# Kernel optimization log

Hardware: AMD Instinct MI355X
Metric: run time of the kernel (lower is better)

Reference implementation:

```python
import jax, jax.numpy as jnp
import numpy as np

D_MODEL = 1024
NUM_HEADS = 16
DEPTH = D_MODEL // NUM_HEADS
B, S = 4, 2048


def setup_inputs() -> dict:
    key = jax.random.key(0)
    ks = jax.random.split(key, 13)
    sd = 1.0 / np.sqrt(D_MODEL)
    inp = {
        "q_in": jax.random.normal(ks[0], (B, S, D_MODEL), jnp.float32),
        "k_in": jax.random.normal(ks[1], (B, S, D_MODEL), jnp.float32),
        "v_in": jax.random.normal(ks[2], (B, S, D_MODEL), jnp.float32),
        # binary padding/causal-style mask: 1 = masked position
        "m_in": (jax.random.uniform(ks[3], (B, 1, S, S)) < 0.1).astype(jnp.float32),
        "Wq": jax.random.normal(ks[4], (D_MODEL, D_MODEL), jnp.float32) * sd,
        "bq": jax.random.normal(ks[5], (D_MODEL,), jnp.float32) * 0.01,
        "Wk": jax.random.normal(ks[6], (D_MODEL, D_MODEL), jnp.float32) * sd,
        "bk": jax.random.normal(ks[7], (D_MODEL,), jnp.float32) * 0.01,
        "Wv": jax.random.normal(ks[8], (D_MODEL, D_MODEL), jnp.float32) * sd,
        "bv": jax.random.normal(ks[9], (D_MODEL,), jnp.float32) * 0.01,
        "Wo": jax.random.normal(ks[10], (D_MODEL, D_MODEL), jnp.float32) * sd,
        "bo": jax.random.normal(ks[11], (D_MODEL,), jnp.float32) * 0.01,
    }
    return inp


def _split(t):
    # [B,S,D] -> [B,H,S,depth]
    b, s, _ = t.shape
    return t.reshape(b, s, NUM_HEADS, DEPTH).transpose(0, 2, 1, 3)


def reference(q_in, k_in, v_in, m_in, Wq, bq, Wk, bk, Wv, bv, Wo, bo):
    # torch Linear: x @ W^T + b
    q = _split(q_in @ Wq.T + bq)
    k = _split(k_in @ Wk.T + bk)
    v = _split(v_in @ Wv.T + bv)
    scale = jnp.sqrt(jnp.asarray(DEPTH, jnp.float32))
    scores = jnp.einsum("bhqd,bhkd->bhqk", q, k) / scale
    scores = scores - m_in * 1e6
    attn = jax.nn.softmax(scores, axis=-1)
    out = jnp.einsum("bhqk,bhkd->bhqd", attn, v)  # [B,H,S,depth]
    out = out.transpose(0, 2, 1, 3).reshape(q_in.shape[0], -1, D_MODEL)
    return out @ Wo.T + bo
```

## Files before the change

kernel.cpp:

```cpp
#include <hip/hip_runtime.h>


typedef __bf16 bf16_t;
typedef __bf16 bf16x4 __attribute__((ext_vector_type(4)));
typedef __bf16 bf16x8 __attribute__((ext_vector_type(8)));
typedef float floatx2 __attribute__((ext_vector_type(2)));
typedef float floatx4 __attribute__((ext_vector_type(4)));
typedef float floatx16 __attribute__((ext_vector_type(16)));

#define DMODEL 1024
#define NHEAD  16
#define DEPTH  64
#define BATCH  4
#define SEQ    2048
#define MROWS  (BATCH * SEQ)

#define QSCALE 0.18033688011112042f

#define GLDS16(gaddr, laddr)                                                   \
  __builtin_amdgcn_global_load_lds(                                            \
      (__attribute__((address_space(1))) void*)(gaddr),                        \
      (__attribute__((address_space(3))) void*)(laddr), 16, 0, 0)

__global__ __launch_bounds__(256) void cvt_weights(
    const float* __restrict__ w0, const float* __restrict__ w1,
    const float* __restrict__ w2, const float* __restrict__ w3,
    bf16_t* __restrict__ out) {
  const int n_per4 = (DMODEL * DMODEL) / 4;
  int idx = blockIdx.x * blockDim.x + threadIdx.x;
  int t = idx / n_per4;
  int e4 = idx - t * n_per4;
  const float* src = (t == 0) ? w0 : (t == 1) ? w1 : (t == 2) ? w2 : w3;
  const float sc = (t == 0) ? QSCALE : 1.0f;
  float4 v = ((const float4*)src)[e4];
  bf16_t* dst = out + (size_t)t * (DMODEL * DMODEL) + (size_t)e4 * 4;
  dst[0] = (bf16_t)(v.x * sc); dst[1] = (bf16_t)(v.y * sc);
  dst[2] = (bf16_t)(v.z * sc); dst[3] = (bf16_t)(v.w * sc);
}

__global__ __launch_bounds__(256) void cvt3(
    const float* __restrict__ q, const float* __restrict__ k,
    const float* __restrict__ v, bf16_t* __restrict__ dst) {
  const size_t n8 = (size_t)MROWS * DMODEL / 8;
  size_t i = (size_t)blockIdx.x * blockDim.x + threadIdx.x;
  int t = (int)(i / n8);
  size_t e = i - (size_t)t * n8;
  const float* src = (t == 0) ? q : (t == 1) ? k : v;
  const float4* s = (const float4*)(src + e * 8);
  float4 f0 = s[0], f1 = s[1];
  bf16x8 o;
  o[0] = (bf16_t)f0.x; o[1] = (bf16_t)f0.y; o[2] = (bf16_t)f0.z; o[3] = (bf16_t)f0.w;
  o[4] = (bf16_t)f1.x; o[5] = (bf16_t)f1.y; o[6] = (bf16_t)f1.z; o[7] = (bf16_t)f1.w;
  *(bf16x8*)(dst + i * 8) = o;
}

__global__ __launch_bounds__(256) void mask_prepack(
    const float* __restrict__ m, unsigned int* __restrict__ M32) {
  size_t t = (size_t)blockIdx.x * blockDim.x + threadIdx.x;
  int lane = (int)(t & 63);
  int it = (int)((t >> 6) & 31);
  int g  = (int)((t >> 11) & 63);
  int b  = (int)(t >> 17);
  int q  = g * 32 + (lane & 31);
  int hi = lane >> 5;
  const float* row = m + ((size_t)b * SEQ + q) * SEQ + it * 64;
  unsigned int bits = 0;
#pragma unroll
  for (int kb = 0; kb < 2; kb++) {
#pragma unroll
    for (int rc = 0; rc < 4; rc++) {
      const int base = kb * 32 + 16 * (rc >> 1) + 8 * hi + 4 * (rc & 1);
      const float4 mv = *(const float4*)(row + base);
      const int bit0 = kb * 16 + rc * 4;
      if (mv.x == 0.f) bits |= 1u << (bit0 + 0);
      if (mv.y == 0.f) bits |= 1u << (bit0 + 1);
      if (mv.z == 0.f) bits |= 1u << (bit0 + 2);
      if (mv.w == 0.f) bits |= 1u << (bit0 + 3);
    }
  }
  M32[t] = bits;
}

__global__ __launch_bounds__(256) void gemm_qkv(
    const bf16_t* __restrict__ Abf3, const bf16_t* __restrict__ Wbf,
    const float* __restrict__ bq, const float* __restrict__ bk,
    const float* __restrict__ bv, bf16_t* __restrict__ Qh,
    bf16_t* __restrict__ Kh, bf16_t* __restrict__ Vth) {
  __shared__ __align__(16) bf16_t As[128 * 64];
  __shared__ __align__(16) bf16_t Bs[128 * 64];
  const int K = DMODEL;
  const int tid = threadIdx.x;
  const int lane = tid & 63;
  const int w = tid >> 6;
  const int quad = lane >> 4;
  const int l16 = lane & 15;
  const int wm = w & 1, wn = w >> 1;
  const int z = blockIdx.z;

  const bf16_t* A = Abf3 + (size_t)z * MROWS * DMODEL;
  const bf16_t* Bt = Wbf + (size_t)z * DMODEL * DMODEL;
  const float* bias = (z == 0) ? bq : (z == 1) ? bk : bv;
  const float bias_scale = (z == 0) ? QSCALE : 1.0f;
  bf16_t* Ov = (z == 0) ? Qh : (z == 1) ? Kh : Vth;

  const int lin = blockIdx.x + 8 * blockIdx.y;
  const int c = lin & 7;
  const int j = lin >> 3;
  const int n0 = (j & 7) * 128;
  const int m0 = ((j >> 3) * 8 + c) * 128;

  const int r8l = lane >> 3;
  const int c8l = (lane & 7) ^ r8l;
  const bf16_t* Ag = A + (size_t)(m0 + w * 32 + r8l) * K + c8l * 8;
  const bf16_t* Bg = Bt + (size_t)(n0 + w * 32 + r8l) * K + c8l * 8;
  char* AsB = (char*)As + (w * 32) * 128;
  char* BsB = (char*)Bs + (w * 32) * 128;

  floatx4 acc[4][4] = {};

  for (int kk = 0; kk < K; kk += 64) {
    __syncthreads();
#pragma unroll
    for (int cl = 0; cl < 4; cl++) {
      GLDS16(Ag + kk + (size_t)(cl * 8) * K, AsB + cl * 8 * 128);
      GLDS16(Bg + kk + (size_t)(cl * 8) * K, BsB + cl * 8 * 128);
    }
    __syncthreads();

#pragma unroll
    for (int kk2 = 0; kk2 < 2; kk2++) {
      bf16x8 af[4], bfr[4];
#pragma unroll
      for (int mi = 0; mi < 4; mi++) {
        const char* Arow = (const char*)As + (wm * 64 + mi * 16 + l16) * 128;
        af[mi] = *(const bf16x8*)(Arow + (((kk2 * 4 + quad) ^ (l16 & 7)) * 16));
      }
#pragma unroll
      for (int ni = 0; ni < 4; ni++) {
        const char* Brow = (const char*)Bs + (wn * 64 + ni * 16 + l16) * 128;
        bfr[ni] = *(const bf16x8*)(Brow + (((kk2 * 4 + quad) ^ (l16 & 7)) * 16));
      }
#pragma unroll
      for (int mi = 0; mi < 4; mi++)
#pragma unroll
        for (int ni = 0; ni < 4; ni++)
          acc[mi][ni] = __builtin_amdgcn_mfma_f32_16x16x32_bf16(af[mi], bfr[ni], acc[mi][ni], 0, 0, 0);
    }
  }

#pragma unroll
  for (int ni = 0; ni < 4; ni++) {
    const int col = n0 + wn * 64 + ni * 16 + l16;
    const float bvl = bias_scale * bias[col];
    const int hh = col >> 6, d = col & (DEPTH - 1);
#pragma unroll
    for (int mi = 0; mi < 4; mi++) {
#pragma unroll
      for (int r = 0; r < 4; r++) {
        const int row = m0 + wm * 64 + mi * 16 + quad * 4 + r;
        const float val = acc[mi][ni][r] + bvl;
        const int bb = row >> 11, s = row & (SEQ - 1);
        if (z != 2) {
          Ov[((((size_t)bb * NHEAD + hh) * SEQ + s) << 6) + d] = (bf16_t)val;
        } else {
          Ov[(((size_t)bb * NHEAD + hh) * DEPTH + d) * SEQ + s] = (bf16_t)val;
        }
      }
    }
  }
}

__global__ __launch_bounds__(256) void gemm_wo(
    const bf16_t* __restrict__ A, const bf16_t* __restrict__ Bt,
    const float* __restrict__ bias, float* __restrict__ Ov,
    int M, int N, int K) {
  __shared__ __align__(16) bf16_t As[128 * 64];
  __shared__ __align__(16) bf16_t Bs[128 * 64];
  const int tid = threadIdx.x;
  const int lane = tid & 63;
  const int w = tid >> 6;
  const int quad = lane >> 4;
  const int l16 = lane & 15;
  const int wm = w & 1, wn = w >> 1;

  const int lin = blockIdx.x + 8 * blockIdx.y;
  const int c = lin & 7;
  const int j = lin >> 3;
  const int n0 = (j & 7) * 128;
  const int m0 = ((j >> 3) * 8 + c) * 128;

  const int r8l = lane >> 3;
  const int c8l = (lane & 7) ^ r8l;
  const bf16_t* Ag = A + (size_t)(m0 + w * 32 + r8l) * K + c8l * 8;
  const bf16_t* Bg = Bt + (size_t)(n0 + w * 32 + r8l) * K + c8l * 8;
  char* AsB = (char*)As + (w * 32) * 128;
  char* BsB = (char*)Bs + (w * 32) * 128;

  floatx4 acc[4][4] = {};

  for (int kk = 0; kk < K; kk += 64) {
    __syncthreads();
#pragma unroll
    for (int cl = 0; cl < 4; cl++) {
      GLDS16(Ag + kk + (size_t)(cl * 8) * K, AsB + cl * 8 * 128);
      GLDS16(Bg + kk + (size_t)(cl * 8) * K, BsB + cl * 8 * 128);
    }
    __syncthreads();

#pragma unroll
    for (int kk2 = 0; kk2 < 2; kk2++) {
      bf16x8 af[4], bfr[4];
#pragma unroll
      for (int mi = 0; mi < 4; mi++) {
        const char* Arow = (const char*)As + (wm * 64 + mi * 16 + l16) * 128;
        af[mi] = *(const bf16x8*)(Arow + (((kk2 * 4 + quad) ^ (l16 & 7)) * 16));
      }
#pragma unroll
      for (int ni = 0; ni < 4; ni++) {
        const char* Brow = (const char*)Bs + (wn * 64 + ni * 16 + l16) * 128;
        bfr[ni] = *(const bf16x8*)(Brow + (((kk2 * 4 + quad) ^ (l16 & 7)) * 16));
      }
#pragma unroll
      for (int mi = 0; mi < 4; mi++)
#pragma unroll
        for (int ni = 0; ni < 4; ni++)
          acc[mi][ni] = __builtin_amdgcn_mfma_f32_16x16x32_bf16(af[mi], bfr[ni], acc[mi][ni], 0, 0, 0);
    }
  }

#pragma unroll
  for (int ni = 0; ni < 4; ni++) {
    const int col = n0 + wn * 64 + ni * 16 + l16;
    const float bv = bias[col];
#pragma unroll
    for (int mi = 0; mi < 4; mi++)
#pragma unroll
      for (int r = 0; r < 4; r++) {
        const int row = m0 + wm * 64 + mi * 16 + quad * 4 + r;
        Ov[(size_t)row * N + col] = acc[mi][ni][r] + bv;
      }
  }
}

__global__ __launch_bounds__(256, 4) void attn_kernel(
    const bf16_t* __restrict__ Qh, const bf16_t* __restrict__ Kh,
    const bf16_t* __restrict__ Vt, const unsigned int* __restrict__ M32,
    bf16_t* __restrict__ O) {
  const int lane = threadIdx.x & 63;
  const int w = __builtin_amdgcn_readfirstlane(threadIdx.x >> 6);
  const int l31 = lane & 31;
  const int hi = lane >> 5;

  const int lin = blockIdx.x + 16 * blockIdx.y + 256 * blockIdx.z;
  const int x8 = lin & 7;
  const int kk = lin >> 3;
  const int qt = kk & 15;
  const int bh = ((kk >> 4) << 3) | x8;
  const int h = bh & 15;
  const int b = bh >> 4;
  const int q0 = qt * 128;

  const bf16_t* Qb = Qh + ((size_t)b * NHEAD + h) * SEQ * DEPTH;
  const bf16_t* Kb = Kh + ((size_t)b * NHEAD + h) * SEQ * DEPTH;
  const bf16_t* Vb = Vt + ((size_t)b * NHEAD + h) * DEPTH * SEQ;
  const unsigned int* Mw =
      M32 + ((size_t)b * 64 + (qt * 4 + w)) * 32 * 64 + lane;

  __shared__ __align__(16) bf16_t Ksm[64 * 64];
  __shared__ __align__(16) bf16_t Vsm[64 * 64];
  __shared__ float Lsm[4][32];

  const int r8 = lane >> 3;
  const int c8 = (lane & 7) ^ r8;
  const int i1 = w * 16 + r8;
  const int i2 = i1 + 8;
  const int lo1 = i1 & 31, lo2 = i2 & 31;
  const int s1 = (i1 & 32) | ((lo1 & ~12) | ((lo1 & 4) << 1) | ((lo1 & 8) >> 1));
  const int s2 = (i2 & 32) | ((lo2 & ~12) | ((lo2 & 4) << 1) | ((lo2 & 8) >> 1));
  const bf16_t* Kg1 = Kb + (size_t)s1 * DEPTH + c8 * 8;
  const bf16_t* Kg2 = Kb + (size_t)s2 * DEPTH + c8 * 8;
  const bf16_t* Vg  = Vb + (size_t)(w * 16 + r8) * SEQ + c8 * 8;
  const int woff = (w * 16) * 128;

  bf16x8 aq[4];
  {
    const bf16_t* qp = Qb + (size_t)(q0 + w * 32 + l31) * DEPTH + hi * 8;
#pragma unroll
    for (int t = 0; t < 4; t++) aq[t] = *(const bf16x8*)(qp + t * 16);
  }

  floatx16 acco[2] = {};
  floatx2 l2 = {0.f, 0.f};
  const int kxor = l31 & 7;

  for (int it = 0; it < SEQ / 64; ++it) {
    const int sk = it * 64;
    const unsigned int mword = Mw[it * 64];
    __syncthreads();
    {
      char* KsB = (char*)Ksm + woff;
      char* VsB = (char*)Vsm + woff;
      GLDS16(Kg1 + (size_t)sk * DEPTH, KsB);
      GLDS16(Kg2 + (size_t)sk * DEPTH, KsB + 8 * 128);
      GLDS16(Vg + sk, VsB);
      GLDS16(Vg + sk + (size_t)8 * SEQ, VsB + 8 * 128);
    }
    __syncthreads();

#pragma unroll
    for (int kb = 0; kb < 2; kb++) {
      floatx16 s = {};
      const char* Krow = (const char*)Ksm + (kb * 32 + l31) * 128;
#pragma unroll
      for (int t = 0; t < 4; t++) {
        bf16x8 kf = *(const bf16x8*)(Krow + (((2 * t + hi) ^ kxor) * 16));
        s = __builtin_amdgcn_mfma_f32_32x32x16_bf16(kf, aq[t], s, 0, 0, 0);
      }
      float pv[16];
#pragma unroll
      for (int r = 0; r < 16; r++) {
        float e = __builtin_amdgcn_exp2f(s[r]);
        const int km = __builtin_amdgcn_sbfe((int)mword, kb * 16 + r, 1);
        pv[r] = __int_as_float(__float_as_int(e) & km);
      }
#pragma unroll
      for (int r = 0; r < 8; r++)
        l2 += (floatx2){pv[2 * r], pv[2 * r + 1]};
#pragma unroll
      for (int mh = 0; mh < 2; mh++) {
        bf16x8 pa;
#pragma unroll
        for (int j2 = 0; j2 < 8; j2++) pa[j2] = (bf16_t)pv[mh * 8 + j2];
        const int m = kb * 2 + mh;
#pragma unroll
        for (int n = 0; n < 2; n++) {
          const char* Vrow = (const char*)Vsm + (n * 32 + l31) * 128;
          bf16x8 vf = *(const bf16x8*)(Vrow + (((2 * m + hi) ^ kxor) * 16));
          acco[n] = __builtin_amdgcn_mfma_f32_32x32x16_bf16(pa, vf, acco[n], 0, 0, 0);
        }
      }
    }
  }

  float lsum = l2.x + l2.y;
  float tot = lsum + __shfl_xor(lsum, 32);
  if (lane < 32) Lsm[w][l31] = __frcp_rn(tot);
  __syncthreads();

#pragma unroll
  for (int r = 0; r < 16; r++) {
    const int qr = (r & 3) + 8 * (r >> 2) + 4 * hi;
    const float inv = Lsm[w][qr];
    const size_t srow = (size_t)q0 + w * 32 + qr;
#pragma unroll
    for (int n = 0; n < 2; n++) {
      const int d = h * DEPTH + n * 32 + l31;
      O[((size_t)b * SEQ + srow) * DMODEL + d] = (bf16_t)(acco[n][r] * inv);
    }
  }
}

extern "C" void kernel_launch(void* const* d_in, const int* in_sizes, int n_in,
                              void* d_out, int out_size, void* d_ws, size_t ws_size,
                              hipStream_t stream) {
  const float* q_in = (const float*)d_in[0];
  const float* k_in = (const float*)d_in[1];
  const float* v_in = (const float*)d_in[2];
  const float* m_in = (const float*)d_in[3];
  const float* Wq = (const float*)d_in[4];
  const float* bq = (const float*)d_in[5];
  const float* Wk = (const float*)d_in[6];
  const float* bk = (const float*)d_in[7];
  const float* Wv = (const float*)d_in[8];
  const float* bv = (const float*)d_in[9];
  const float* Wo = (const float*)d_in[10];
  const float* bo = (const float*)d_in[11];

  char* ws = (char*)d_ws;
  const size_t MB = 1024 * 1024;
  bf16_t* wbf  = (bf16_t*)ws;
  bf16_t* Abf3 = (bf16_t*)(ws + 8 * MB);
  bf16_t* Obuf = (bf16_t*)(ws + 8 * MB);
  bf16_t* Qh   = (bf16_t*)(ws + 56 * MB);
  bf16_t* Kh   = (bf16_t*)(ws + 72 * MB);
  bf16_t* Vth  = (bf16_t*)(ws + 88 * MB);
  unsigned int* M32 = (unsigned int*)(ws + 104 * MB);

  cvt_weights<<<(4 * (DMODEL * DMODEL / 4)) / 256, 256, 0, stream>>>(
      Wq, Wk, Wv, Wo, wbf);
  cvt3<<<(3 * (MROWS * DMODEL / 8)) / 256, 256, 0, stream>>>(
      q_in, k_in, v_in, Abf3);
  mask_prepack<<<(BATCH * 64 * 32 * 64) / 256, 256, 0, stream>>>(m_in, M32);

  dim3 gqkv(8, 64, 3);
  gemm_qkv<<<gqkv, 256, 0, stream>>>(Abf3, wbf, bq, bk, bv, Qh, Kh, Vth);

  dim3 ga(SEQ / 128, NHEAD, BATCH);
  attn_kernel<<<ga, 256, 0, stream>>>(Qh, Kh, Vth, M32, Obuf);

  dim3 gg(8, 64);
  gemm_wo<<<gg, 256, 0, stream>>>(
      Obuf, wbf + 3 * (size_t)DMODEL * DMODEL, bo, (float*)d_out,
      MROWS, DMODEL, DMODEL);
}
```

Before: 405.3 us.

## Fuse fp32-to-bf16 activation conversion into QKV GEMM tile loads

Removes the separate cvt3 kernel that converted q/k/v activations to bf16. The QKV GEMM now loads fp32 A tiles directly into LDS through global_load_lds with an XOR swizzle and converts to bf16 in registers before the MFMA. This saves a full write and re-read of the bf16 activation buffer plus one kernel launch. In exchange the A tile doubles LDS footprint and traffic, and conversion work is repeated once per N-tile block (8 times per A element).

Measured after the change: 414.3 us. +2.2%, slower.

```diff
diff --git a/kernel.cpp b/kernel.cpp
--- a/kernel.cpp
+++ b/kernel.cpp
@@ -38,22 +38,6 @@
   dst[2] = (bf16_t)(v.z * sc); dst[3] = (bf16_t)(v.w * sc);
 }
 
-__global__ __launch_bounds__(256) void cvt3(
-    const float* __restrict__ q, const float* __restrict__ k,
-    const float* __restrict__ v, bf16_t* __restrict__ dst) {
-  const size_t n8 = (size_t)MROWS * DMODEL / 8;
-  size_t i = (size_t)blockIdx.x * blockDim.x + threadIdx.x;
-  int t = (int)(i / n8);
-  size_t e = i - (size_t)t * n8;
-  const float* src = (t == 0) ? q : (t == 1) ? k : v;
-  const float4* s = (const float4*)(src + e * 8);
-  float4 f0 = s[0], f1 = s[1];
-  bf16x8 o;
-  o[0] = (bf16_t)f0.x; o[1] = (bf16_t)f0.y; o[2] = (bf16_t)f0.z; o[3] = (bf16_t)f0.w;
-  o[4] = (bf16_t)f1.x; o[5] = (bf16_t)f1.y; o[6] = (bf16_t)f1.z; o[7] = (bf16_t)f1.w;
-  *(bf16x8*)(dst + i * 8) = o;
-}
-
 __global__ __launch_bounds__(256) void mask_prepack(
     const float* __restrict__ m, unsigned int* __restrict__ M32) {
   size_t t = (size_t)blockIdx.x * blockDim.x + threadIdx.x;
@@ -82,11 +66,12 @@
 }
 
 __global__ __launch_bounds__(256) void gemm_qkv(
-    const bf16_t* __restrict__ Abf3, const bf16_t* __restrict__ Wbf,
+    const float* __restrict__ Aq, const float* __restrict__ Ak,
+    const float* __restrict__ Av, const bf16_t* __restrict__ Wbf,
     const float* __restrict__ bq, const float* __restrict__ bk,
     const float* __restrict__ bv, bf16_t* __restrict__ Qh,
     bf16_t* __restrict__ Kh, bf16_t* __restrict__ Vth) {
-  __shared__ __align__(16) bf16_t As[128 * 64];
+  __shared__ __align__(16) float  Asf[128 * 64];
   __shared__ __align__(16) bf16_t Bs[128 * 64];
   const int K = DMODEL;
   const int tid = threadIdx.x;
@@ -97,7 +82,7 @@
   const int wm = w & 1, wn = w >> 1;
   const int z = blockIdx.z;
 
-  const bf16_t* A = Abf3 + (size_t)z * MROWS * DMODEL;
+  const float* A = (z == 0) ? Aq : (z == 1) ? Ak : Av;
   const bf16_t* Bt = Wbf + (size_t)z * DMODEL * DMODEL;
   const float* bias = (z == 0) ? bq : (z == 1) ? bk : bv;
   const float bias_scale = (z == 0) ? QSCALE : 1.0f;
@@ -109,11 +94,19 @@
   const int n0 = (j & 7) * 128;
   const int m0 = ((j >> 3) * 8 + c) * 128;
 
+  const int c16 = lane & 15;
+  const int r4 = lane >> 4;
+  const float* AgP[8];
+#pragma unroll
+  for (int cl = 0; cl < 8; cl++) {
+    const int lr = w * 32 + cl * 4 + r4;
+    const int cs = c16 ^ ((cl * 4 + r4) & 15);
+    AgP[cl] = A + (size_t)(m0 + lr) * K + cs * 4;
+  }
   const int r8l = lane >> 3;
   const int c8l = (lane & 7) ^ r8l;
-  const bf16_t* Ag = A + (size_t)(m0 + w * 32 + r8l) * K + c8l * 8;
   const bf16_t* Bg = Bt + (size_t)(n0 + w * 32 + r8l) * K + c8l * 8;
-  char* AsB = (char*)As + (w * 32) * 128;
+  char* AsB = (char*)Asf + (w * 32) * 256;
   char* BsB = (char*)Bs + (w * 32) * 128;
 
   floatx4 acc[4][4] = {};
@@ -121,10 +114,11 @@
   for (int kk = 0; kk < K; kk += 64) {
     __syncthreads();
 #pragma unroll
-    for (int cl = 0; cl < 4; cl++) {
-      GLDS16(Ag + kk + (size_t)(cl * 8) * K, AsB + cl * 8 * 128);
+    for (int cl = 0; cl < 8; cl++)
+      GLDS16(AgP[cl] + kk, AsB + cl * 1024);
+#pragma unroll
+    for (int cl = 0; cl < 4; cl++)
       GLDS16(Bg + kk + (size_t)(cl * 8) * K, BsB + cl * 8 * 128);
-    }
     __syncthreads();
 
 #pragma unroll
@@ -132,8 +126,15 @@
       bf16x8 af[4], bfr[4];
 #pragma unroll
       for (int mi = 0; mi < 4; mi++) {
-        const char* Arow = (const char*)As + (wm * 64 + mi * 16 + l16) * 128;
-        af[mi] = *(const bf16x8*)(Arow + (((kk2 * 4 + quad) ^ (l16 & 7)) * 16));
+        const char* Arow = (const char*)Asf + (wm * 64 + mi * 16 + l16) * 256;
+        const int cg = kk2 * 8 + quad * 2;
+        floatx4 a0 = *(const floatx4*)(Arow + ((cg ^ l16) * 16));
+        floatx4 a1 = *(const floatx4*)(Arow + (((cg + 1) ^ l16) * 16));
+#pragma unroll
+        for (int e = 0; e < 4; e++) {
+          af[mi][e] = (bf16_t)a0[e];
+          af[mi][4 + e] = (bf16_t)a1[e];
+        }
       }
 #pragma unroll
       for (int ni = 0; ni < 4; ni++) {
@@ -379,7 +380,6 @@
   char* ws = (char*)d_ws;
   const size_t MB = 1024 * 1024;
   bf16_t* wbf  = (bf16_t*)ws;
-  bf16_t* Abf3 = (bf16_t*)(ws + 8 * MB);
   bf16_t* Obuf = (bf16_t*)(ws + 8 * MB);
   bf16_t* Qh   = (bf16_t*)(ws + 56 * MB);
   bf16_t* Kh   = (bf16_t*)(ws + 72 * MB);
@@ -388,12 +388,11 @@
 
   cvt_weights<<<(4 * (DMODEL * DMODEL / 4)) / 256, 256, 0, stream>>>(
       Wq, Wk, Wv, Wo, wbf);
-  cvt3<<<(3 * (MROWS * DMODEL / 8)) / 256, 256, 0, stream>>>(
-      q_in, k_in, v_in, Abf3);
   mask_prepack<<<(BATCH * 64 * 32 * 64) / 256, 256, 0, stream>>>(m_in, M32);
 
   dim3 gqkv(8, 64, 3);
-  gemm_qkv<<<gqkv, 256, 0, stream>>>(Abf3, wbf, bq, bk, bv, Qh, Kh, Vth);
+  gemm_qkv<<<gqkv, 256, 0, stream>>>(q_in, k_in, v_in, wbf, bq, bk, bv,
+                                     Qh, Kh, Vth);
 
   dim3 ga(SEQ / 128, NHEAD, BATCH);
   attn_kernel<<<ga, 256, 0, stream>>>(Qh, Kh, Vth, M32, Obuf);
```
